# Kernel optimization log

Hardware: AMD Instinct MI355X
Metric: run time of the kernel (lower is better)

Reference implementation:

```python
import jax, jax.numpy as jnp
import numpy as np

RADIUS_VIEWPOOL = 0.075  # self.view_pool_radius
EPS_BN = 1e-5


def _pconv(x, w, b):
    # 1x1 Conv1d: x (B, Cin, N), w (Cout, Cin), b (Cout,)
    return jnp.einsum('oc,bcn->bon', w, x) + b[None, :, None]


def _bn(x, p):
    # eval-mode BatchNorm1d; p rows: gamma, beta, running_mean, running_var
    g, b, m, v = p[0], p[1], p[2], p[3]
    inv = g * jax.lax.rsqrt(v + EPS_BN)
    return (x - m[None, :, None]) * inv[None, :, None] + b[None, :, None]


def setup_inputs() -> dict:
    key = jax.random.key(0)
    it = iter(jax.random.split(key, 80))
    Np, Nr = 16384, 8192
    inp = {}
    inp['pcd_xyz'] = jax.random.uniform(next(it), (1, Np, 3), jnp.float32)
    inp['rgb_xyz'] = jax.random.uniform(next(it), (1, Nr, 3), jnp.float32)
    inp['pcd_features'] = jax.random.normal(next(it), (1, 32, Np), jnp.float32)
    inp['rgb_features'] = jax.random.normal(next(it), (1, 128, Nr), jnp.float32)

    def conv(name, o, c):
        s = 1.0 / np.sqrt(c)
        inp[name + '_w'] = jax.random.uniform(next(it), (o, c), jnp.float32, -s, s)
        inp[name + '_b'] = jax.random.uniform(next(it), (o,), jnp.float32, -s, s)

    def bn(name, c):
        g = 1.0 + 0.1 * jax.random.normal(next(it), (c,), jnp.float32)
        b = 0.1 * jax.random.normal(next(it), (c,), jnp.float32)
        m = 0.1 * jax.random.normal(next(it), (c,), jnp.float32)
        v = jax.random.uniform(next(it), (c,), jnp.float32, 0.5, 1.5)
        inp[name] = jnp.stack([g, b, m, v])

    conv('cc1', 384, 384); bn('cc_bn', 384); conv('cc2', 128, 384)
    conv('co1', 256, 256); bn('co_bn', 256); conv('co2', 128, 256)
    conv('dh1', 160, 160); bn('dh1_bn', 160)
    conv('dh2', 160, 160); bn('dh2_bn', 160)
    conv('dh3', 128, 160)
    conv('sh1', 128, 128); bn('sh_bn', 128)
    conv('sh2', 1, 128)
    return inp


def _forward(pcd_xyz, rgb_xyz, pcd_features, rgb_features,
             cc1_w, cc1_b, cc_bn, cc2_w, cc2_b,
             co1_w, co1_b, co_bn, co2_w, co2_b,
             dh1_w, dh1_b, dh1_bn, dh2_w, dh2_b, dh2_bn, dh3_w, dh3_b,
             sh1_w, sh1_b, sh_bn, sh2_w, sh2_b):
    Np = pcd_xyz.shape[1]
    Nr = rgb_xyz.shape[1]
    C_rgb = rgb_features.shape[1]

    # ---- three_nn: 3 nearest rgb points for each pcd point ----
    d2 = jnp.sum((pcd_xyz[0, :, None, :] - rgb_xyz[0, None, :, :]) ** 2, axis=-1)  # (Np, Nr)
    neg_d2, idx = jax.lax.top_k(-d2, 3)                     # (Np, 3)
    dist = jnp.sqrt(jnp.maximum(-neg_d2, 0.0))
    # idx[dist > radius] = -1 in torch -> indexes shadow (zero) row appended at end
    neighbor = jnp.where(dist > RADIUS_VIEWPOOL, Nr, idx)   # (Np, 3)

    rgb_f = jnp.concatenate([rgb_features[0].T,
                             jnp.zeros((1, C_rgb), rgb_features.dtype)], axis=0)  # (Nr+1, 128)
    nf = rgb_f[neighbor]                                    # (Np, 3, 128) gather
    max_features = nf.max(axis=1)                           # (Np, 128)

    # fuception fusion: conv over concatenated neighbor features, then fuse with max
    x_cat = nf.reshape(Np, 3 * C_rgb).T[None]               # (1, 384, Np)
    h = jax.nn.relu(_bn(_pconv(x_cat, cc1_w, cc1_b), cc_bn))
    concat_out = _pconv(h, cc2_w, cc2_b)                    # (1, 128, Np)
    x2 = jnp.concatenate([concat_out, max_features.T[None]], axis=1)  # (1, 256, Np)
    h = jax.nn.relu(_bn(_pconv(x2, co1_w, co1_b), co_bn))
    attach = _pconv(h, co2_w, co2_b)                        # (1, 128, Np)

    # fuse pcd + assigned rgb features -> direct feature header (160 = 128+32)
    full = jnp.concatenate([pcd_features, attach], axis=1)  # (1, 160, Np)
    h = jax.nn.relu(_bn(_pconv(full, dh1_w, dh1_b), dh1_bn))
    h = jax.nn.relu(_bn(_pconv(h, dh2_w, dh2_b), dh2_bn))
    fp = _pconv(h, dh3_w, dh3_b)                            # (1, 128, Np)

    # score header: conv-bn-relu-conv-sigmoid
    s = jax.nn.relu(_bn(_pconv(fp, sh1_w, sh1_b), sh_bn))
    vote_scores = jax.nn.sigmoid(_pconv(s, sh2_w, sh2_b))[0, 0]  # (Np,)

    # L2-normalized vote features (N, 128)
    vf = fp[0].T
    vf = vf / jnp.maximum(jnp.linalg.norm(vf, axis=1, keepdims=True), 1e-12)
    return pcd_xyz[0], vote_scores, vf


def reference(pcd_xyz, rgb_xyz, pcd_features, rgb_features,
              cc1_w, cc1_b, cc_bn, cc2_w, cc2_b,
              co1_w, co1_b, co_bn, co2_w, co2_b,
              dh1_w, dh1_b, dh1_bn, dh2_w, dh2_b, dh2_bn, dh3_w, dh3_b,
              sh1_w, sh1_b, sh_bn, sh2_w, sh2_b):
    return _forward(pcd_xyz, rgb_xyz, pcd_features, rgb_features,
                    cc1_w, cc1_b, cc_bn, cc2_w, cc2_b,
                    co1_w, co1_b, co_bn, co2_w, co2_b,
                    dh1_w, dh1_b, dh1_bn, dh2_w, dh2_b, dh2_bn, dh3_w, dh3_b,
                    sh1_w, sh1_b, sh_bn, sh2_w, sh2_b)
```

## Files before the change

kernel.cpp:

```cpp
#include <hip/hip_runtime.h>
#include <math.h>

#define NP 16384
#define NR 8192
#define GRID 13
#define NCELL (GRID * GRID * GRID)
#define CAP 28

typedef __attribute__((ext_vector_type(8))) short short8;
typedef __attribute__((ext_vector_type(4))) float f32x4;

__device__ inline unsigned short f2b(float f) {
  unsigned int x = __float_as_uint(f);
  return (unsigned short)((x + 0x7FFFu + ((x >> 16) & 1u)) >> 16);
}
__device__ inline float blo(unsigned int u) { return __uint_as_float(u << 16); }
__device__ inline float bhi(unsigned int u) { return __uint_as_float(u & 0xffff0000u); }

__global__ __launch_bounds__(256) void k_pre(const float* __restrict__ rf,
                                             const float* __restrict__ rxyz,
                                             const float* __restrict__ pf,
                                             const float* __restrict__ s0, const float* __restrict__ s1,
                                             const float* __restrict__ s2, const float* __restrict__ s3,
                                             const float* __restrict__ s4, const float* __restrict__ s5,
                                             const float* __restrict__ s6, const float* __restrict__ s7,
                                             unsigned short* __restrict__ rgbTb,
                                             float4* __restrict__ rxyz4,
                                             unsigned short* __restrict__ fullp,
                                             unsigned short* __restrict__ dst,
                                             int* __restrict__ cellCnt) {
  __shared__ float tile[128][65];
  int b = blockIdx.x, t = threadIdx.x;
  if (b < 128) {
    int r0 = b * 64;
    for (int e = 0; e < 32; ++e) {
      int idx = t + e * 256;
      int c = idx >> 6, rl = idx & 63;
      tile[c][rl] = rf[c * NR + r0 + rl];
    }
    __syncthreads();
    for (int e = 0; e < 32; ++e) {
      int idx = t + e * 256;
      int rl = idx >> 7, c = idx & 127;
      rgbTb[(size_t)(r0 + rl) * 128 + c] = f2b(tile[c][rl]);
    }
    if (b == 0 && t < 128) rgbTb[(size_t)NR * 128 + t] = 0;
    if ((t >> 6) == 0) {
      int i = r0 + (t & 63);
      float x = rxyz[i * 3], y = rxyz[i * 3 + 1], z = rxyz[i * 3 + 2];
      rxyz4[i] = make_float4(x, y, z, 0.f);
    }
  } else if (b < 384) {
    int n0 = (b - 128) * 64;
    for (int e = 0; e < 8; ++e) {
      int idx = t + e * 256;
      int c = idx >> 6, nl = idx & 63;
      tile[c][nl] = pf[c * NP + n0 + nl];
    }
    __syncthreads();
    for (int e = 0; e < 8; ++e) {
      int idx = t + e * 256;
      int nl = idx >> 5, c = idx & 31;
      fullp[(size_t)(n0 + nl) * 32 + c] = f2b(tile[c][nl]);
    }
  } else if (b < 960) {
    const int groups[8] = {18432, 6144, 8192, 4096, 3200, 3200, 2560, 2048};
    const int Cs[8]     = {384, 384, 256, 256, 160, 160, 160, 128};
    const int offs[8]   = {0, 147456, 196608, 262144, 294912, 320512, 346112, 366592};
    const float* srcs[8] = {s0, s1, s2, s3, s4, s5, s6, s7};
    int j = b - 384;
    int m = j / 72, bx = j % 72;
    int gidx = bx * 256 + t;
    if (gidx >= groups[m]) return;
    int C = Cs[m], NC = C >> 5;
    int ot = gidx / (NC * 64);
    int rem = gidx - ot * (NC * 64);
    int k = rem >> 6, lane = rem & 63;
    int q = lane >> 4, l15 = lane & 15;
    const float* sp = srcs[m] + (size_t)(ot * 16 + l15) * C + k * 32 + q * 8;
    float4 a = *(const float4*)sp, c4 = *(const float4*)(sp + 4);
    uint4 o;
    o.x = f2b(a.x) | ((unsigned int)f2b(a.y) << 16);
    o.y = f2b(a.z) | ((unsigned int)f2b(a.w) << 16);
    o.z = f2b(c4.x) | ((unsigned int)f2b(c4.y) << 16);
    o.w = f2b(c4.z) | ((unsigned int)f2b(c4.w) << 16);
    *(uint4*)(dst + offs[m] + (size_t)gidx * 8) = o;
  } else {
    int idx = (b - 960) * 256 + t;
    if (idx < NCELL) cellCnt[idx] = 0;
  }
}

__global__ __launch_bounds__(64) void k_build(const float4* __restrict__ rxyz4,
                                              int* __restrict__ cellCnt,
                                              float4* __restrict__ cellTab) {
  int i = blockIdx.x * 64 + threadIdx.x;
  float4 r = rxyz4[i];
  int cx = (int)(r.x * 13.f); cx = cx < 0 ? 0 : (cx > 12 ? 12 : cx);
  int cy = (int)(r.y * 13.f); cy = cy < 0 ? 0 : (cy > 12 ? 12 : cy);
  int cz = (int)(r.z * 13.f); cz = cz < 0 ? 0 : (cz > 12 ? 12 : cz);
  int cell = (cz * 13 + cy) * 13 + cx;
  int slot = atomicAdd(&cellCnt[cell], 1);
  if (slot < CAP) cellTab[(size_t)cell * CAP + slot] = make_float4(r.x, r.y, r.z, __int_as_float(i));
}

__global__ __launch_bounds__(256) void k_nn_grid(const float* __restrict__ pxyz,
                                                 const int* __restrict__ cellCnt,
                                                 const float4* __restrict__ cellTab,
                                                 int* __restrict__ nbr) {
  int tid = blockIdx.x * 256 + threadIdx.x;
  int n = tid >> 5, l32 = tid & 31;
  float px = pxyz[n * 3], py = pxyz[n * 3 + 1], pz = pxyz[n * 3 + 2];
  int cx = (int)(px * 13.f); cx = cx < 0 ? 0 : (cx > 12 ? 12 : cx);
  int cy = (int)(py * 13.f); cy = cy < 0 ? 0 : (cy > 12 ? 12 : cy);
  int cz = (int)(pz * 13.f); cz = cz < 0 ? 0 : (cz > 12 ? 12 : cz);
  const float R2L = 0.005626125f;
  const unsigned long long SENT = ((unsigned long long)__float_as_uint(R2L) << 32);
  unsigned long long k0 = SENT, k1 = SENT, k2 = SENT;
  if (l32 < 27) {
    int dz = l32 / 9 - 1, dy = (l32 / 3) % 3 - 1, dx = l32 % 3 - 1;
    int zz = cz + dz, yy = cy + dy, xx = cx + dx;
    if ((unsigned)zz <= 12u && (unsigned)yy <= 12u && (unsigned)xx <= 12u) {
      int c = (zz * 13 + yy) * 13 + xx;
      int m = cellCnt[c]; m = m < CAP ? m : CAP;
      const float4* tp = cellTab + (size_t)c * CAP;
      for (int k = 0; k < m; ++k) {
        float4 qq = tp[k];
        float dxx = qq.x - px, dyy = qq.y - py, dzz = qq.z - pz;
        float d2 = fmaf(dxx, dxx, fmaf(dyy, dyy, dzz * dzz));
        unsigned long long key =
            ((unsigned long long)__float_as_uint(d2) << 32) | (unsigned int)__float_as_int(qq.w);
        if (key < k2) {
          if (key < k1) {
            k2 = k1;
            if (key < k0) { k1 = k0; k0 = key; }
            else          { k1 = key; }
          } else k2 = key;
        }
      }
    }
  }
  int pos = 0;
  unsigned long long res[3];
#pragma unroll
  for (int r = 0; r < 3; ++r) {
    unsigned long long cur = (pos == 0) ? k0 : (pos == 1) ? k1 : (pos == 2) ? k2 : ~0ull;
    unsigned long long m = cur;
#pragma unroll
    for (int o = 1; o <= 16; o <<= 1) {
      unsigned long long other = __shfl_xor(m, o);
      m = other < m ? other : m;
    }
    res[r] = m;
    if (cur == m) ++pos;
  }
  if (l32 == 0) {
    const float R2 = 0.075f * 0.075f;
    float d0 = __uint_as_float((unsigned int)(res[0] >> 32));
    float d1 = __uint_as_float((unsigned int)(res[1] >> 32));
    float d2v = __uint_as_float((unsigned int)(res[2] >> 32));
    int j0 = (d0 > R2) ? NR : (int)(res[0] & 0xffffffffu);
    int j1 = (d1 > R2) ? NR : (int)(res[1] & 0xffffffffu);
    int j2 = (d2v > R2) ? NR : (int)(res[2] & 0xffffffffu);
    nbr[n * 3 + 0] = j0; nbr[n * 3 + 1] = j1; nbr[n * 3 + 2] = j2;
  }
}

template <int C, int O, int COFF, bool BN, bool RELU>
__device__ __forceinline__ void mlp_layer(const unsigned short* __restrict__ W,
                                          const float* __restrict__ bias,
                                          const float* __restrict__ bnp,
                                          const unsigned short* Xs,
                                          unsigned short* Ys,
                                          int wo, int q, int l15, int lane) {
  constexpr int NC = C / 32;
  constexpr int NT = O / 16;
  constexpr int MT = (NT + 7) / 8;
  f32x4 acc[MT][2];
  short8 afb[2][MT];
  const unsigned short* wp[MT];
#pragma unroll
  for (int i = 0; i < MT; ++i) {
    acc[i][0] = (f32x4){0.f, 0.f, 0.f, 0.f};
    acc[i][1] = (f32x4){0.f, 0.f, 0.f, 0.f};
    int ot = wo + i * 8;
    wp[i] = W + ((size_t)(((ot < NT) ? ot : 0) * NC) * 64 + lane) * 8;
  }
#pragma unroll
  for (int k = 0; k < 2 && k < NC; ++k)
#pragma unroll
    for (int i = 0; i < MT; ++i)
      if (wo + i * 8 < NT) afb[k][i] = *(const short8*)(wp[i] + (size_t)k * 512);
  short8 bf0 = *(const short8*)&Xs[l15 * 392 + q * 8];
  short8 bf1 = *(const short8*)&Xs[(16 + l15) * 392 + q * 8];
#pragma unroll
  for (int k = 0; k < NC; ++k) {
    short8 nbf0 = bf0, nbf1 = bf1;
    if (k + 1 < NC) {
      nbf0 = *(const short8*)&Xs[l15 * 392 + (k + 1) * 32 + q * 8];
      nbf1 = *(const short8*)&Xs[(16 + l15) * 392 + (k + 1) * 32 + q * 8];
    }
    int slot = k & 1;
#pragma unroll
    for (int i = 0; i < MT; ++i) {
      if (wo + i * 8 < NT) {
        acc[i][0] = __builtin_amdgcn_mfma_f32_16x16x32_bf16(afb[slot][i], bf0, acc[i][0], 0, 0, 0);
        acc[i][1] = __builtin_amdgcn_mfma_f32_16x16x32_bf16(afb[slot][i], bf1, acc[i][1], 0, 0, 0);
      }
    }
    if (k + 2 < NC) {
#pragma unroll
      for (int i = 0; i < MT; ++i)
        if (wo + i * 8 < NT) afb[slot][i] = *(const short8*)(wp[i] + (size_t)(k + 2) * 512);
    }
    bf0 = nbf0; bf1 = nbf1;
  }
#pragma unroll
  for (int i = 0; i < MT; ++i) {
    int ot = wo + i * 8;
    if (ot >= NT) continue;
    int o4 = ot * 16 + q * 4;
    f32x4 bb = *(const f32x4*)(bias + o4);
    f32x4 sc, sh;
    if (BN) {
      f32x4 g  = *(const f32x4*)(bnp + o4);
      f32x4 be = *(const f32x4*)(bnp + O + o4);
      f32x4 mm = *(const f32x4*)(bnp + 2 * O + o4);
      f32x4 vv = *(const f32x4*)(bnp + 3 * O + o4);
#pragma unroll
      for (int r = 0; r < 4; ++r) {
        float inv = g[r] * rsqrtf(vv[r] + 1e-5f);
        sc[r] = inv; sh[r] = (bb[r] - mm[r]) * inv + be[r];
      }
    } else {
      sc = (f32x4){1.f, 1.f, 1.f, 1.f}; sh = bb;
    }
#pragma unroll
    for (int rt = 0; rt < 2; ++rt) {
      ushort4 u;
#pragma unroll
      for (int r = 0; r < 4; ++r) {
        float x = acc[i][rt][r] * sc[r] + sh[r];
        if (RELU) x = fmaxf(x, 0.f);
        ((unsigned short*)&u)[r] = f2b(x);
      }
      *(ushort4*)&Ys[(rt * 16 + l15) * 392 + COFF + ot * 16 + q * 4] = u;
    }
  }
}

__global__ __launch_bounds__(512) void k_mlp(
    const unsigned short* __restrict__ rgbTb,
    const int* __restrict__ nbr,
    const unsigned short* __restrict__ fullp,
    const unsigned short* __restrict__ wcc1, const unsigned short* __restrict__ wcc2,
    const unsigned short* __restrict__ wco1, const unsigned short* __restrict__ wco2,
    const unsigned short* __restrict__ wdh1, const unsigned short* __restrict__ wdh2,
    const unsigned short* __restrict__ wdh3, const unsigned short* __restrict__ wsh1,
    const float* __restrict__ cc1_b, const float* __restrict__ cc_bn,
    const float* __restrict__ cc2_b,
    const float* __restrict__ co1_b, const float* __restrict__ co_bn,
    const float* __restrict__ co2_b,
    const float* __restrict__ dh1_b, const float* __restrict__ dh1_bn,
    const float* __restrict__ dh2_b, const float* __restrict__ dh2_bn,
    const float* __restrict__ dh3_b,
    const float* __restrict__ sh1_b, const float* __restrict__ sh_bn,
    const float* __restrict__ sh2_w, const float* __restrict__ sh2_b,
    const float* __restrict__ pxyz, float* __restrict__ out) {
  __shared__ unsigned short Ab[32 * 392];
  __shared__ unsigned short Bb[32 * 392];
  int t = threadIdx.x, lane = t & 63, w = t >> 6;
  int wo = w & 7;
  int q = lane >> 4, l15 = lane & 15;
  int n0 = blockIdx.x * 32;
  unsigned int mreg[4];
#pragma unroll
  for (int pj = 0; pj < 4; ++pj) {
    int r = w * 4 + pj;
    int n = n0 + r;
    unsigned int j0 = (unsigned int)nbr[n * 3 + 0]; j0 = j0 > NR ? NR : j0;
    unsigned int j1 = (unsigned int)nbr[n * 3 + 1]; j1 = j1 > NR ? NR : j1;
    unsigned int j2 = (unsigned int)nbr[n * 3 + 2]; j2 = j2 > NR ? NR : j2;
    unsigned int a = ((const unsigned int*)(rgbTb + (size_t)j0 * 128))[lane];
    unsigned int b = ((const unsigned int*)(rgbTb + (size_t)j1 * 128))[lane];
    unsigned int c = ((const unsigned int*)(rgbTb + (size_t)j2 * 128))[lane];
    unsigned int* xr = (unsigned int*)&Ab[r * 392];
    xr[lane] = a; xr[64 + lane] = b; xr[128 + lane] = c;
    float ml = fmaxf(blo(a), fmaxf(blo(b), blo(c)));
    float mh = fmaxf(bhi(a), fmaxf(bhi(b), bhi(c)));
    mreg[pj] = (__float_as_uint(mh) & 0xffff0000u) | (__float_as_uint(ml) >> 16);
  }
  __syncthreads();
  mlp_layer<384, 384, 0, true,  true >(wcc1, cc1_b, cc_bn, Ab, Bb, wo, q, l15, lane);
  __syncthreads();
#pragma unroll
  for (int pj = 0; pj < 4; ++pj)
    ((unsigned int*)&Ab[(w * 4 + pj) * 392])[64 + lane] = mreg[pj];
  mlp_layer<384, 128, 0, false, false>(wcc2, cc2_b, nullptr, Bb, Ab, wo, q, l15, lane);
  __syncthreads();
  mlp_layer<256, 256, 0, true,  true >(wco1, co1_b, co_bn, Ab, Bb, wo, q, l15, lane);
  __syncthreads();
  mlp_layer<256, 128, 32, false, false>(wco2, co2_b, nullptr, Bb, Ab, wo, q, l15, lane);
  for (int idx = t; idx < 128; idx += 512) {
    int row = idx >> 2, c8 = idx & 3;
    *(uint4*)&Ab[row * 392 + c8 * 8] = *(const uint4*)(fullp + (size_t)(n0 + row) * 32 + c8 * 8);
  }
  __syncthreads();
  mlp_layer<160, 160, 0, true,  true >(wdh1, dh1_b, dh1_bn, Ab, Bb, wo, q, l15, lane);
  __syncthreads();
  mlp_layer<160, 160, 0, true,  true >(wdh2, dh2_b, dh2_bn, Bb, Ab, wo, q, l15, lane);
  __syncthreads();
  mlp_layer<160, 128, 0, false, false>(wdh3, dh3_b, nullptr, Ab, Bb, wo, q, l15, lane);
  __syncthreads();
  mlp_layer<128, 128, 0, true,  true >(wsh1, sh1_b, sh_bn, Bb, Ab, wo, q, l15, lane);
  __syncthreads();
  int col8 = (lane & 15) * 8;
  float4 w0 = *(const float4*)(sh2_w + col8);
  float4 wA = *(const float4*)(sh2_w + col8 + 4);
  float bvv = sh2_b[0];
  int row = w * 4 + (lane >> 4);
  uint4 raw = *(const uint4*)&Ab[row * 392 + col8];
  float acc = blo(raw.x) * w0.x + bhi(raw.x) * w0.y + blo(raw.y) * w0.z + bhi(raw.y) * w0.w +
              blo(raw.z) * wA.x + bhi(raw.z) * wA.y + blo(raw.w) * wA.z + bhi(raw.w) * wA.w;
  acc += __shfl_xor(acc, 1); acc += __shfl_xor(acc, 2);
  acc += __shfl_xor(acc, 4); acc += __shfl_xor(acc, 8);
  if ((lane & 15) == 0) out[49152 + n0 + row] = 1.f / (1.f + expf(-(acc + bvv)));
  uint4 rf = *(const uint4*)&Bb[row * 392 + col8];
  float v[8] = {blo(rf.x), bhi(rf.x), blo(rf.y), bhi(rf.y),
                blo(rf.z), bhi(rf.z), blo(rf.w), bhi(rf.w)};
  float s = 0.f;
#pragma unroll
  for (int i = 0; i < 8; ++i) s = fmaf(v[i], v[i], s);
  s += __shfl_xor(s, 1); s += __shfl_xor(s, 2);
  s += __shfl_xor(s, 4); s += __shfl_xor(s, 8);
  float inv = 1.f / fmaxf(sqrtf(s), 1e-12f);
  float* op = out + 65536 + (size_t)(n0 + row) * 128 + col8;
  *(float4*)op = make_float4(v[0] * inv, v[1] * inv, v[2] * inv, v[3] * inv);
  *(float4*)(op + 4) = make_float4(v[4] * inv, v[5] * inv, v[6] * inv, v[7] * inv);
  for (int i = t; i < 96; i += 512) out[n0 * 3 + i] = pxyz[n0 * 3 + i];
}

extern "C" void kernel_launch(void* const* d_in, const int* in_sizes, int n_in,
                              void* d_out, int out_size, void* d_ws, size_t ws_size,
                              hipStream_t stream) {
  const float* pcd_xyz = (const float*)d_in[0];
  const float* rgb_xyz = (const float*)d_in[1];
  const float* pcd_f   = (const float*)d_in[2];
  const float* rgb_f   = (const float*)d_in[3];
  const float* cc1_w = (const float*)d_in[4];  const float* cc1_b = (const float*)d_in[5];
  const float* cc_bn = (const float*)d_in[6];
  const float* cc2_w = (const float*)d_in[7];  const float* cc2_b = (const float*)d_in[8];
  const float* co1_w = (const float*)d_in[9];  const float* co1_b = (const float*)d_in[10];
  const float* co_bn = (const float*)d_in[11];
  const float* co2_w = (const float*)d_in[12]; const float* co2_b = (const float*)d_in[13];
  const float* dh1_w = (const float*)d_in[14]; const float* dh1_b = (const float*)d_in[15];
  const float* dh1_bn = (const float*)d_in[16];
  const float* dh2_w = (const float*)d_in[17]; const float* dh2_b = (const float*)d_in[18];
  const float* dh2_bn = (const float*)d_in[19];
  const float* dh3_w = (const float*)d_in[20]; const float* dh3_b = (const float*)d_in[21];
  const float* sh1_w = (const float*)d_in[22]; const float* sh1_b = (const float*)d_in[23];
  const float* sh_bn = (const float*)d_in[24];
  const float* sh2_w = (const float*)d_in[25]; const float* sh2_b = (const float*)d_in[26];

  char* ws = (char*)d_ws;
  float* out = (float*)d_out;

  unsigned short* wb    = (unsigned short*)(ws);
  unsigned short* rgbTb = (unsigned short*)(ws + 0x100000);
  float4* rxyz4         = (float4*)(ws + 0x320000);
  int*    nbr           = (int*)(ws + 0x400000);
  int*    cellCnt       = (int*)(ws + 0x480000);
  float4* cellTab       = (float4*)(ws + 0x490000);
  unsigned short* fullp = (unsigned short*)(ws + 0xA00000);

  unsigned short* wb_cc1 = wb;
  unsigned short* wb_cc2 = wb + 147456;
  unsigned short* wb_co1 = wb + 196608;
  unsigned short* wb_co2 = wb + 262144;
  unsigned short* wb_dh1 = wb + 294912;
  unsigned short* wb_dh2 = wb + 320512;
  unsigned short* wb_dh3 = wb + 346112;
  unsigned short* wb_sh1 = wb + 366592;

  k_pre<<<969, 256, 0, stream>>>(rgb_f, rgb_xyz, pcd_f,
                                 cc1_w, cc2_w, co1_w, co2_w, dh1_w, dh2_w, dh3_w, sh1_w,
                                 rgbTb, rxyz4, fullp, wb, cellCnt);
  k_build<<<128, 64, 0, stream>>>(rxyz4, cellCnt, cellTab);
  k_nn_grid<<<2048, 256, 0, stream>>>(pcd_xyz, cellCnt, cellTab, nbr);
  k_mlp<<<512, 512, 0, stream>>>(rgbTb, nbr, fullp,
                                 wb_cc1, wb_cc2, wb_co1, wb_co2,
                                 wb_dh1, wb_dh2, wb_dh3, wb_sh1,
                                 cc1_b, cc_bn, cc2_b, co1_b, co_bn, co2_b,
                                 dh1_b, dh1_bn, dh2_b, dh2_bn, dh3_b,
                                 sh1_b, sh_bn, sh2_w, sh2_b,
                                 pcd_xyz, out);
}
```

Baseline: 157.1 us.

## Fuse grid nearest-neighbour search into MLP kernel prologue

Removes the separate k_nn_grid launch and does the 3-NN grid search at the start of k_mlp. Each 16-lane group handles one point and walks up to two of the 27 neighbour cells per lane, then reduces with a 16-wide shuffle and writes the indices to shared memory. This drops one kernel launch and the global round trip of the neighbour indices. In exchange, each lane does more serial cell scanning and the MLP waves stall until the search finishes, with only 512 blocks to hide the latency.

```diff
diff --git a/kernel.cpp b/kernel.cpp
--- a/kernel.cpp
+++ b/kernel.cpp
@@ -104,68 +104,6 @@
   if (slot < CAP) cellTab[(size_t)cell * CAP + slot] = make_float4(r.x, r.y, r.z, __int_as_float(i));
 }
 
-__global__ __launch_bounds__(256) void k_nn_grid(const float* __restrict__ pxyz,
-                                                 const int* __restrict__ cellCnt,
-                                                 const float4* __restrict__ cellTab,
-                                                 int* __restrict__ nbr) {
-  int tid = blockIdx.x * 256 + threadIdx.x;
-  int n = tid >> 5, l32 = tid & 31;
-  float px = pxyz[n * 3], py = pxyz[n * 3 + 1], pz = pxyz[n * 3 + 2];
-  int cx = (int)(px * 13.f); cx = cx < 0 ? 0 : (cx > 12 ? 12 : cx);
-  int cy = (int)(py * 13.f); cy = cy < 0 ? 0 : (cy > 12 ? 12 : cy);
-  int cz = (int)(pz * 13.f); cz = cz < 0 ? 0 : (cz > 12 ? 12 : cz);
-  const float R2L = 0.005626125f;
-  const unsigned long long SENT = ((unsigned long long)__float_as_uint(R2L) << 32);
-  unsigned long long k0 = SENT, k1 = SENT, k2 = SENT;
-  if (l32 < 27) {
-    int dz = l32 / 9 - 1, dy = (l32 / 3) % 3 - 1, dx = l32 % 3 - 1;
-    int zz = cz + dz, yy = cy + dy, xx = cx + dx;
-    if ((unsigned)zz <= 12u && (unsigned)yy <= 12u && (unsigned)xx <= 12u) {
-      int c = (zz * 13 + yy) * 13 + xx;
-      int m = cellCnt[c]; m = m < CAP ? m : CAP;
-      const float4* tp = cellTab + (size_t)c * CAP;
-      for (int k = 0; k < m; ++k) {
-        float4 qq = tp[k];
-        float dxx = qq.x - px, dyy = qq.y - py, dzz = qq.z - pz;
-        float d2 = fmaf(dxx, dxx, fmaf(dyy, dyy, dzz * dzz));
-        unsigned long long key =
-            ((unsigned long long)__float_as_uint(d2) << 32) | (unsigned int)__float_as_int(qq.w);
-        if (key < k2) {
-          if (key < k1) {
-            k2 = k1;
-            if (key < k0) { k1 = k0; k0 = key; }
-            else          { k1 = key; }
-          } else k2 = key;
-        }
-      }
-    }
-  }
-  int pos = 0;
-  unsigned long long res[3];
-#pragma unroll
-  for (int r = 0; r < 3; ++r) {
-    unsigned long long cur = (pos == 0) ? k0 : (pos == 1) ? k1 : (pos == 2) ? k2 : ~0ull;
-    unsigned long long m = cur;
-#pragma unroll
-    for (int o = 1; o <= 16; o <<= 1) {
-      unsigned long long other = __shfl_xor(m, o);
-      m = other < m ? other : m;
-    }
-    res[r] = m;
-    if (cur == m) ++pos;
-  }
-  if (l32 == 0) {
-    const float R2 = 0.075f * 0.075f;
-    float d0 = __uint_as_float((unsigned int)(res[0] >> 32));
-    float d1 = __uint_as_float((unsigned int)(res[1] >> 32));
-    float d2v = __uint_as_float((unsigned int)(res[2] >> 32));
-    int j0 = (d0 > R2) ? NR : (int)(res[0] & 0xffffffffu);
-    int j1 = (d1 > R2) ? NR : (int)(res[1] & 0xffffffffu);
-    int j2 = (d2v > R2) ? NR : (int)(res[2] & 0xffffffffu);
-    nbr[n * 3 + 0] = j0; nbr[n * 3 + 1] = j1; nbr[n * 3 + 2] = j2;
-  }
-}
-
 template <int C, int O, int COFF, bool BN, bool RELU>
 __device__ __forceinline__ void mlp_layer(const unsigned short* __restrict__ W,
                                           const float* __restrict__ bias,
@@ -251,7 +189,9 @@
 
 __global__ __launch_bounds__(512) void k_mlp(
     const unsigned short* __restrict__ rgbTb,
-    const int* __restrict__ nbr,
+    const float* __restrict__ pxyz,
+    const int* __restrict__ cellCnt,
+    const float4* __restrict__ cellTab,
     const unsigned short* __restrict__ fullp,
     const unsigned short* __restrict__ wcc1, const unsigned short* __restrict__ wcc2,
     const unsigned short* __restrict__ wco1, const unsigned short* __restrict__ wco2,
@@ -266,21 +206,78 @@
     const float* __restrict__ dh3_b,
     const float* __restrict__ sh1_b, const float* __restrict__ sh_bn,
     const float* __restrict__ sh2_w, const float* __restrict__ sh2_b,
-    const float* __restrict__ pxyz, float* __restrict__ out) {
+    float* __restrict__ out) {
   __shared__ unsigned short Ab[32 * 392];
   __shared__ unsigned short Bb[32 * 392];
+  __shared__ int nbrS[32][3];
   int t = threadIdx.x, lane = t & 63, w = t >> 6;
   int wo = w & 7;
   int q = lane >> 4, l15 = lane & 15;
   int n0 = blockIdx.x * 32;
+  {
+    int n = n0 + w * 4 + q;
+    float px = pxyz[n * 3], py = pxyz[n * 3 + 1], pz = pxyz[n * 3 + 2];
+    int cx = (int)(px * 13.f); cx = cx < 0 ? 0 : (cx > 12 ? 12 : cx);
+    int cy = (int)(py * 13.f); cy = cy < 0 ? 0 : (cy > 12 ? 12 : cy);
+    int cz = (int)(pz * 13.f); cz = cz < 0 ? 0 : (cz > 12 ? 12 : cz);
+    const float R2L = 0.005626125f;
+    const unsigned long long SENT = ((unsigned long long)__float_as_uint(R2L) << 32);
+    unsigned long long k0 = SENT, k1 = SENT, k2 = SENT;
+    for (int ci = l15; ci < 27; ci += 16) {
+      int dz = ci / 9 - 1, dyc = (ci / 3) % 3 - 1, dxc = ci % 3 - 1;
+      int zz = cz + dz, yy = cy + dyc, xx = cx + dxc;
+      if ((unsigned)zz <= 12u && (unsigned)yy <= 12u && (unsigned)xx <= 12u) {
+        int c = (zz * 13 + yy) * 13 + xx;
+        int m = cellCnt[c]; m = m < CAP ? m : CAP;
+        const float4* tp = cellTab + (size_t)c * CAP;
+        for (int k = 0; k < m; ++k) {
+          float4 qq = tp[k];
+          float dxx = qq.x - px, dyy = qq.y - py, dzz = qq.z - pz;
+          float d2 = fmaf(dxx, dxx, fmaf(dyy, dyy, dzz * dzz));
+          unsigned long long key =
+              ((unsigned long long)__float_as_uint(d2) << 32) | (unsigned int)__float_as_int(qq.w);
+          if (key < k2) {
+            if (key < k1) {
+              k2 = k1;
+              if (key < k0) { k1 = k0; k0 = key; }
+              else          { k1 = key; }
+            } else k2 = key;
+          }
+        }
+      }
+    }
+    int pos = 0;
+    unsigned long long res[3];
+#pragma unroll
+    for (int r = 0; r < 3; ++r) {
+      unsigned long long cur = (pos == 0) ? k0 : (pos == 1) ? k1 : (pos == 2) ? k2 : ~0ull;
+      unsigned long long m = cur;
+#pragma unroll
+      for (int o = 1; o <= 8; o <<= 1) {
+        unsigned long long other = __shfl_xor(m, o);
+        m = other < m ? other : m;
+      }
+      res[r] = m;
+      if (cur == m) ++pos;
+    }
+    if (l15 == 0) {
+      const float R2 = 0.075f * 0.075f;
+      float d0 = __uint_as_float((unsigned int)(res[0] >> 32));
+      float d1 = __uint_as_float((unsigned int)(res[1] >> 32));
+      float d2v = __uint_as_float((unsigned int)(res[2] >> 32));
+      nbrS[w * 4 + q][0] = (d0 > R2) ? NR : (int)(res[0] & 0xffffffffu);
+      nbrS[w * 4 + q][1] = (d1 > R2) ? NR : (int)(res[1] & 0xffffffffu);
+      nbrS[w * 4 + q][2] = (d2v > R2) ? NR : (int)(res[2] & 0xffffffffu);
+    }
+  }
+  __syncthreads();
   unsigned int mreg[4];
 #pragma unroll
   for (int pj = 0; pj < 4; ++pj) {
     int r = w * 4 + pj;
-    int n = n0 + r;
-    unsigned int j0 = (unsigned int)nbr[n * 3 + 0]; j0 = j0 > NR ? NR : j0;
-    unsigned int j1 = (unsigned int)nbr[n * 3 + 1]; j1 = j1 > NR ? NR : j1;
-    unsigned int j2 = (unsigned int)nbr[n * 3 + 2]; j2 = j2 > NR ? NR : j2;
+    unsigned int j0 = (unsigned int)nbrS[r][0]; j0 = j0 > NR ? NR : j0;
+    unsigned int j1 = (unsigned int)nbrS[r][1]; j1 = j1 > NR ? NR : j1;
+    unsigned int j2 = (unsigned int)nbrS[r][2]; j2 = j2 > NR ? NR : j2;
     unsigned int a = ((const unsigned int*)(rgbTb + (size_t)j0 * 128))[lane];
     unsigned int b = ((const unsigned int*)(rgbTb + (size_t)j1 * 128))[lane];
     unsigned int c = ((const unsigned int*)(rgbTb + (size_t)j2 * 128))[lane];
@@ -368,7 +365,6 @@
   unsigned short* wb    = (unsigned short*)(ws);
   unsigned short* rgbTb = (unsigned short*)(ws + 0x100000);
   float4* rxyz4         = (float4*)(ws + 0x320000);
-  int*    nbr           = (int*)(ws + 0x400000);
   int*    cellCnt       = (int*)(ws + 0x480000);
   float4* cellTab       = (float4*)(ws + 0x490000);
   unsigned short* fullp = (unsigned short*)(ws + 0xA00000);
@@ -386,12 +382,11 @@
                                  cc1_w, cc2_w, co1_w, co2_w, dh1_w, dh2_w, dh3_w, sh1_w,
                                  rgbTb, rxyz4, fullp, wb, cellCnt);
   k_build<<<128, 64, 0, stream>>>(rxyz4, cellCnt, cellTab);
-  k_nn_grid<<<2048, 256, 0, stream>>>(pcd_xyz, cellCnt, cellTab, nbr);
-  k_mlp<<<512, 512, 0, stream>>>(rgbTb, nbr, fullp,
+  k_mlp<<<512, 512, 0, stream>>>(rgbTb, pcd_xyz, cellCnt, cellTab, fullp,
                                  wb_cc1, wb_cc2, wb_co1, wb_co2,
                                  wb_dh1, wb_dh2, wb_dh3, wb_sh1,
                                  cc1_b, cc_bn, cc2_b, co1_b, co_bn, co2_b,
                                  dh1_b, dh1_bn, dh2_b, dh2_bn, dh3_b,
                                  sh1_b, sh_bn, sh2_w, sh2_b,
-                                 pcd_xyz, out);
-}
+                                 out);
+}
```

After: 152.9 us (median of 2 runs). 1.03x faster.
